# Kernel optimization log

Measured on AMD Instinct MI355X. Metric: run time of the kernel, lower is better.

## Reference

```python
import jax, jax.numpy as jnp
import numpy as np

B, T, N, E = 4, 32, 370, 11840
H, HEADS, DH, L, K = 64, 4, 16, 3, 5

def gelu(x):
    return jax.nn.gelu(x, approximate=False)  # torch default GELU is exact erf

def setup_inputs() -> dict:
    key = jax.random.key(0)
    ks = jax.random.split(key, 18)
    s = 0.05  # keep activations well-scaled
    return {
        "x": jax.random.normal(ks[0], (B, T, N, H), jnp.float32),
        "edge_index": jax.random.randint(ks[1], (2, E), 0, N, dtype=jnp.int32),
        "edge_weight": jax.random.uniform(ks[2], (E,), jnp.float32),
        "W_gcn": jax.random.normal(ks[3], (L, H, H), jnp.float32) * s,
        "b_gcn": jax.random.normal(ks[4], (L, H), jnp.float32) * s,
        "W_gat": jax.random.normal(ks[5], (L, H, HEADS * DH), jnp.float32) * s,
        "att_src": jax.random.normal(ks[6], (L, HEADS, DH), jnp.float32) * s,
        "att_dst": jax.random.normal(ks[7], (L, HEADS, DH), jnp.float32) * s,
        "b_gat": jax.random.normal(ks[8], (L, HEADS * DH), jnp.float32) * s,
        "W_t": jax.random.normal(ks[9], (L, H, H, K), jnp.float32) * s,  # (O,I,K)
        "b_t": jax.random.normal(ks[10], (L, H), jnp.float32) * s,
        "ln_g": jnp.ones((L, H), jnp.float32),
        "ln_b": jnp.zeros((L, H), jnp.float32),
        "W1": jax.random.normal(ks[11], (N * H, 256), jnp.float32) * s,
        "b1": jax.random.normal(ks[12], (256,), jnp.float32) * s,
        "W2": jax.random.normal(ks[13], (256, 64), jnp.float32) * s,
        "b2": jax.random.normal(ks[14], (64,), jnp.float32) * s,
    }

def reference(x, edge_index, edge_weight, W_gcn, b_gcn, W_gat, att_src, att_dst,
              b_gat, W_t, b_t, ln_g, ln_b, W1, b1, W2, b2):
    Bb, Tt, Nn, Ff = x.shape
    G = Bb * Tt
    nL = W_gcn.shape[0]
    heads, dh = att_src.shape[1], att_src.shape[2]
    Hh = heads * dh
    # shared topology across all G graphs; add self-loops (PyG default, fill=1.0)
    src, dst = edge_index[0], edge_index[1]
    loop = jnp.arange(Nn, dtype=src.dtype)
    src2 = jnp.concatenate([src, loop])
    dst2 = jnp.concatenate([dst, loop])
    ew2 = jnp.concatenate([edge_weight, jnp.ones((Nn,), edge_weight.dtype)])
    # symmetric GCN normalization (same for every graph in the batch)
    deg = jnp.zeros((Nn,), x.dtype).at[dst2].add(ew2)
    dis = jnp.where(deg > 0, jax.lax.rsqrt(deg), jnp.zeros_like(deg))
    gnorm = dis[src2] * ew2 * dis[dst2]                       # (E2,)
    h = x.reshape(G, Nn, Ff)
    for l in range(nL):
        # ---- GCNConv: transform -> gather -> weighted scatter-add ----
        hw = h @ W_gcn[l]                                     # (G,N,H)
        msg = hw[:, src2] * gnorm[None, :, None]              # (G,E2,H)
        g = jnp.zeros_like(hw).at[:, dst2].add(msg) + b_gcn[l]
        g = gelu(g)
        # ---- GATConv: per-edge softmax attention over incoming edges ----
        gh = (g @ W_gat[l]).reshape(G, Nn, heads, dh)
        asrc = (gh * att_src[l]).sum(-1)                      # (G,N,heads)
        adst = (gh * att_dst[l]).sum(-1)
        e = jax.nn.leaky_relu(asrc[:, src2] + adst[:, dst2], negative_slope=0.2)
        m = jnp.full((G, Nn, heads), -jnp.inf, e.dtype).at[:, dst2].max(e)
        ex = jnp.exp(e - m[:, dst2])
        den = jnp.zeros((G, Nn, heads), e.dtype).at[:, dst2].add(ex)
        alpha = ex / den[:, dst2]                             # (G,E2,heads)
        msgs = gh[:, src2] * alpha[..., None]                 # (G,E2,heads,dh)
        out = jnp.zeros_like(gh).at[:, dst2].add(msgs).reshape(G, Nn, Hh) + b_gat[l]
        # ---- residual + LayerNorm ----
        r = out + h[..., :Hh]
        mu = r.mean(-1, keepdims=True)
        var = ((r - mu) ** 2).mean(-1, keepdims=True)
        h = (r - mu) * jax.lax.rsqrt(var + 1e-5) * ln_g[l] + ln_b[l]
    # ---- temporal convs over T per (batch, node) ----
    Hc = h.shape[-1]
    xt = h.reshape(Bb, Tt, Nn, Hc).transpose(0, 2, 3, 1).reshape(Bb * Nn, Hc, Tt)
    for l in range(nL):
        c = jax.lax.conv_general_dilated(
            xt, W_t[l], (1,), "SAME", dimension_numbers=("NCH", "OIH", "NCH"))
        xt = gelu(c + b_t[l][None, :, None]) + xt
    z = xt.reshape(Bb, Nn, Hc, Tt).transpose(0, 3, 1, 2).reshape(Bb, Tt, Nn * Hc)
    return gelu(z @ W1 + b1) @ W2 + b2
```

## Files before the change

### kernel.cpp

```cpp
#include <hip/hip_runtime.h>
#include <hip/hip_bf16.h>

#define B_   4
#define T_   32
#define N_   370
#define NP_  384
#define E_   11840
#define E2_  12210
#define H_   64
#define G_   128
#define GN_  47360
#define BN_  1480
#define NH_  23680
#define ECAP 320
#define KCH_ 128
#define NCH_ 185

typedef __hip_bfloat16 bf;
typedef short short8 __attribute__((ext_vector_type(8)));
typedef float f32x4 __attribute__((ext_vector_type(4)));

__device__ __forceinline__ float gelu_f(float x){
  return 0.5f * x * (1.0f + erff(x * 0.7071067811865475f));
}
__device__ __forceinline__ float lrelu(float v){ return v > 0.f ? v : 0.2f * v; }
__device__ __forceinline__ float b2f(bf x){ return __bfloat162float(x); }
__device__ __forceinline__ void store_bf4(bf* p, float4 v){
  bf tmp[4] = {__float2bfloat16(v.x), __float2bfloat16(v.y),
               __float2bfloat16(v.z), __float2bfloat16(v.w)};
  *(ushort4*)p = *(const ushort4*)tmp;
}
__device__ __forceinline__ unsigned pk_bf2(float a, float b){
  bf lo = __float2bfloat16(a), hi = __float2bfloat16(b);
  return (unsigned)*(unsigned short*)&lo | ((unsigned)*(unsigned short*)&hi << 16);
}
__device__ __forceinline__ void load_bf8(const bf* p, float* v){
  uint4 u = *(const uint4*)p;
  unsigned ua[4] = {u.x, u.y, u.z, u.w};
  #pragma unroll
  for (int i = 0; i < 4; ++i){
    v[2*i]   = __uint_as_float(ua[i] << 16);
    v[2*i+1] = __uint_as_float(ua[i] & 0xffff0000u);
  }
}

__global__ __launch_bounds__(1024) void k_degscan(const int* __restrict__ ei,
    const float* __restrict__ ew, float* __restrict__ degG,
    int* __restrict__ offs, int* __restrict__ cursor){
  __shared__ float degS[512];
  __shared__ int cntS[512];
  int tid = threadIdx.x;
  if (tid < 512){ degS[tid] = 0.f; cntS[tid] = 0; }
  __syncthreads();
  for (int e = tid; e < E2_; e += 1024){
    int dst = (e < E_) ? ei[E_ + e] : (e - E_);
    float w = (e < E_) ? ew[e] : 1.0f;
    atomicAdd(&degS[dst], w);
    atomicAdd(&cntS[dst], 1);
  }
  __syncthreads();
  if (tid < N_) degG[tid] = degS[tid];
  if (tid < 64){
    int lane = tid;
    int run = 0;
    for (int c0 = 0; c0 < N_; c0 += 64){
      int n = c0 + lane;
      int v = (n < N_) ? cntS[n] : 0;
      int s = v;
      #pragma unroll
      for (int m = 1; m < 64; m <<= 1){
        int t = __shfl_up(s, m, 64);
        if (lane >= m) s += t;
      }
      int excl = run + s - v;
      if (n < N_){ offs[n] = excl; cursor[n] = excl; }
      run += __shfl(s, 63, 64);
    }
    if (lane == 0) offs[N_] = run;
  }
}

__global__ void k_gfa(const int* __restrict__ ei, const float* __restrict__ ew,
                      const float* __restrict__ deg, int* __restrict__ cursor,
                      int* __restrict__ csr_soff, float* __restrict__ A32){
  int e = blockIdx.x * 256 + threadIdx.x;
  if (e >= E2_) return;
  int s = (e < E_) ? ei[e] : (e - E_);
  int d = (e < E_) ? ei[E_ + e] : (e - E_);
  float w = (e < E_) ? ew[e] : 1.0f;
  float ds = deg[s] > 0.f ? rsqrtf(deg[s]) : 0.f;
  float dd = deg[d] > 0.f ? rsqrtf(deg[d]) : 0.f;
  float gn = ds * w * dd;
  int pos = atomicAdd(&cursor[d], 1);
  csr_soff[pos] = s << 13;
  atomicAdd(&A32[d * NP_ + s], gn);
}

__global__ void k_prep(const float* __restrict__ A32, bf* __restrict__ A16,
                       const float* __restrict__ W_gcn, const float* __restrict__ W_gat,
                       bf* __restrict__ WT, const float* __restrict__ Wt,
                       bf* __restrict__ WB){
  int b = blockIdx.x;
  if (b < 144){
    int i = b * 256 + threadIdx.x;
    float4 v = *(const float4*)&A32[i * 4];
    store_bf4(&A16[i * 4], v);
  } else if (b < 240){
    int i = (b - 144) * 256 + threadIdx.x;
    int ci = i & 63;
    int co = (i >> 6) & 63;
    int m  = (i >> 12) & 1;
    int l  = i >> 13;
    const float* W = m ? W_gat : W_gcn;
    WT[i] = __float2bfloat16(W[(size_t)(l * 64 + ci) * 64 + co]);
  } else {
    int i = (b - 240) * 256 + threadIdx.x;
    int j = i & 7;
    int r = i >> 3;
    int lane = r & 63;
    int mi = (r >> 6) & 3;
    int t2 = r >> 8;
    int kk = t2 % 10, l = t2 / 10;
    int ho = mi * 16 + (lane & 15);
    int k  = kk >> 1;
    int ci = (kk & 1) * 32 + (lane >> 4) * 8 + j;
    WB[i] = __float2bfloat16(Wt[((l * 64 + ho) * 64 + ci) * 5 + k]);
  }
}

__global__ __launch_bounds__(256) void k_gcn_dense(const float* __restrict__ hin,
    const bf* __restrict__ A16, const bf* __restrict__ WT,
    const float* __restrict__ b_gcn, const float* __restrict__ att_s,
    const float* __restrict__ att_d, bf* __restrict__ gh16,
    float* __restrict__ asrc, float* __restrict__ adst){
  __shared__ bf As[64 * 136];
  __shared__ bf Bs[64 * 136];
  __shared__ bf Ws1[64 * 72];
  __shared__ bf Ws2[64 * 72];
  __shared__ bf ts[64 * 72];
  int tid = threadIdx.x;
  int b0 = blockIdx.x;
  int xcd = b0 & 7, jj6 = b0 >> 3;
  int g = xcd * 16 + jj6 / 6;
  int m0 = (jj6 % 6) * 64;
  {
    int u = tid & 7, r0w = tid >> 3;
    #pragma unroll
    for (int it = 0; it < 2; ++it){
      int r = r0w + it * 32;
      *(uint4*)&Ws1[r * 72 + u * 8] = *(const uint4*)&WT[(size_t)r * 64 + u * 8];
      *(uint4*)&Ws2[r * 72 + u * 8] = *(const uint4*)&WT[(size_t)(64 + r) * 64 + u * 8];
    }
  }
  int lane = tid & 63, w = tid >> 6;
  int lr = lane & 15, lg = lane >> 4;
  f32x4 acc[4];
  #pragma unroll
  for (int nt = 0; nt < 4; ++nt){ f32x4 zv = {0.f,0.f,0.f,0.f}; acc[nt] = zv; }
  for (int kc = 0; kc < 3; ++kc){
    int u = tid & 15, r = tid >> 4;
    #pragma unroll
    for (int it = 0; it < 4; ++it){
      int row = it * 16 + r;
      *(uint4*)&As[row * 136 + u * 8] =
          *(const uint4*)&A16[(size_t)(m0 + row) * NP_ + kc * 128 + u * 8];
    }
    #pragma unroll
    for (int it = 0; it < 4; ++it){
      int nn = (it * 16 + r) * 2;
      int n = kc * 128 + nn;
      float4 v0 = (n < N_) ? *(const float4*)&hin[((size_t)g * N_ + n) * 64 + u * 4]
                           : make_float4(0.f, 0.f, 0.f, 0.f);
      float4 v1 = (n + 1 < N_) ? *(const float4*)&hin[((size_t)g * N_ + n + 1) * 64 + u * 4]
                               : make_float4(0.f, 0.f, 0.f, 0.f);
      float a0[4] = {v0.x, v0.y, v0.z, v0.w};
      float a1[4] = {v1.x, v1.y, v1.z, v1.w};
      #pragma unroll
      for (int q = 0; q < 4; ++q)
        *(unsigned*)&Bs[(u * 4 + q) * 136 + nn] = pk_bf2(a0[q], a1[q]);
    }
    __syncthreads();
    #pragma unroll
    for (int ks = 0; ks < 4; ++ks){
      short8 af = *(const short8*)&As[(w * 16 + lr) * 136 + ks * 32 + lg * 8];
      #pragma unroll
      for (int nt = 0; nt < 4; ++nt){
        short8 bfr = *(const short8*)&Bs[(nt * 16 + lr) * 136 + ks * 32 + lg * 8];
        acc[nt] = __builtin_amdgcn_mfma_f32_16x16x32_bf16(af, bfr, acc[nt], 0, 0, 0);
      }
    }
    __syncthreads();
  }
  #pragma unroll
  for (int nt = 0; nt < 4; ++nt)
    #pragma unroll
    for (int q = 0; q < 4; ++q)
      ts[(w * 16 + lg * 4 + q) * 72 + nt * 16 + lr] = __float2bfloat16(acc[nt][q]);
  f32x4 acc2[4];
  #pragma unroll
  for (int nt = 0; nt < 4; ++nt){ f32x4 zv = {0.f,0.f,0.f,0.f}; acc2[nt] = zv; }
  #pragma unroll
  for (int ks = 0; ks < 2; ++ks){
    short8 af = *(const short8*)&ts[(w * 16 + lr) * 72 + ks * 32 + lg * 8];
    #pragma unroll
    for (int nt = 0; nt < 4; ++nt){
      short8 bfr = *(const short8*)&Ws1[(nt * 16 + lr) * 72 + ks * 32 + lg * 8];
      acc2[nt] = __builtin_amdgcn_mfma_f32_16x16x32_bf16(af, bfr, acc2[nt], 0, 0, 0);
    }
  }
  #pragma unroll
  for (int nt = 0; nt < 4; ++nt){
    float bv = b_gcn[nt * 16 + lr];
    #pragma unroll
    for (int q = 0; q < 4; ++q){
      float gv = gelu_f(acc2[nt][q] + bv);
      ts[(w * 16 + lg * 4 + q) * 72 + nt * 16 + lr] = __float2bfloat16(gv);
    }
  }
  f32x4 acc3[4];
  #pragma unroll
  for (int nt = 0; nt < 4; ++nt){ f32x4 zv = {0.f,0.f,0.f,0.f}; acc3[nt] = zv; }
  #pragma unroll
  for (int ks = 0; ks < 2; ++ks){
    short8 af = *(const short8*)&ts[(w * 16 + lr) * 72 + ks * 32 + lg * 8];
    #pragma unroll
    for (int nt = 0; nt < 4; ++nt){
      short8 bfr = *(const short8*)&Ws2[(nt * 16 + lr) * 72 + ks * 32 + lg * 8];
      acc3[nt] = __builtin_amdgcn_mfma_f32_16x16x32_bf16(af, bfr, acc3[nt], 0, 0, 0);
    }
  }
  #pragma unroll
  for (int nt = 0; nt < 4; ++nt){
    float sa = att_s[nt * 16 + lr];
    float sd = att_d[nt * 16 + lr];
    float ps[4], pd[4];
    #pragma unroll
    for (int q = 0; q < 4; ++q){
      int n = m0 + w * 16 + lg * 4 + q;
      if (n < N_)
        gh16[((size_t)n * G_ + g) * 64 + nt * 16 + lr] = __float2bfloat16(acc3[nt][q]);
      ps[q] = acc3[nt][q] * sa;
      pd[q] = acc3[nt][q] * sd;
    }
    #pragma unroll
    for (int q = 0; q < 4; ++q){
      ps[q] += __shfl_xor(ps[q], 1, 64); ps[q] += __shfl_xor(ps[q], 2, 64);
      ps[q] += __shfl_xor(ps[q], 4, 64); ps[q] += __shfl_xor(ps[q], 8, 64);
      pd[q] += __shfl_xor(pd[q], 1, 64); pd[q] += __shfl_xor(pd[q], 2, 64);
      pd[q] += __shfl_xor(pd[q], 4, 64); pd[q] += __shfl_xor(pd[q], 8, 64);
    }
    if (lr == 0){
      #pragma unroll
      for (int q = 0; q < 4; ++q){
        int n = m0 + w * 16 + lg * 4 + q;
        if (n < N_){
          asrc[((size_t)n * G_ + g) * 4 + nt] = ps[q];
          adst[((size_t)n * G_ + g) * 4 + nt] = pd[q];
        }
      }
    }
  }
}

__global__ __launch_bounds__(256) void k_gat_agg(const bf* __restrict__ gh,
    const float* __restrict__ asrc, const float* __restrict__ adst,
    const int* __restrict__ csr_soff, const int* __restrict__ offs,
    const float* __restrict__ b_gat, const float* __restrict__ ln_g,
    const float* __restrict__ ln_b, const float* __restrict__ hin,
    float* __restrict__ hout){
  __shared__ int sS[ECAP];
  int b0 = blockIdx.x;
  int gg = (b0 & 7) >> 1;
  int n = (b0 >> 3) * 2 + (b0 & 1);
  int tid = threadIdx.x;
  int o0 = offs[n], o1 = offs[n + 1];
  int deg = o1 - o0;
  int cap = deg < ECAP ? deg : ECAP;
  for (int i = tid; i < cap; i += 256) sS[i] = csr_soff[o0 + i];
  __syncthreads();
  int ql = tid >> 3, c8 = tid & 7;
  int g = gg * 32 + ql;
  int head = c8 >> 1;
  int gh4 = g * 4 + head;
  int toff = gg * 2048 + ql * 64 + c8 * 8;
  float adv = adst[n * 512 + gh4];
  float den = 0.f;
  float a[8];
  #pragma unroll
  for (int j = 0; j < 8; ++j) a[j] = 0.f;
  int p = 0;
  for (; p + 2 <= cap; p += 2){
    int s0 = sS[p], s1 = sS[p+1];
    float w0 = __expf(lrelu(asrc[(s0 >> 4) + gh4] + adv));
    float w1 = __expf(lrelu(asrc[(s1 >> 4) + gh4] + adv));
    den += w0 + w1;
    float v0[8], v1[8];
    load_bf8(gh + s0 + toff, v0);
    load_bf8(gh + s1 + toff, v1);
    #pragma unroll
    for (int j = 0; j < 8; ++j) a[j] += w0 * v0[j] + w1 * v1[j];
  }
  for (; p < cap; ++p){
    int sv = sS[p];
    float w0 = __expf(lrelu(asrc[(sv >> 4) + gh4] + adv));
    den += w0;
    float v[8];
    load_bf8(gh + sv + toff, v);
    #pragma unroll
    for (int j = 0; j < 8; ++j) a[j] += w0 * v[j];
  }
  for (int r = cap; r < deg; ++r){
    int sv = csr_soff[o0 + r];
    float w0 = __expf(lrelu(asrc[(sv >> 4) + gh4] + adv));
    den += w0;
    float v[8];
    load_bf8(gh + sv + toff, v);
    #pragma unroll
    for (int j = 0; j < 8; ++j) a[j] += w0 * v[j];
  }
  float inv = 1.f / den;
  float4 bg0 = *(const float4*)&b_gat[c8 * 8];
  float4 bg1 = *(const float4*)&b_gat[c8 * 8 + 4];
  float bb[8] = {bg0.x, bg0.y, bg0.z, bg0.w, bg1.x, bg1.y, bg1.z, bg1.w};
  size_t hbase = ((size_t)g * N_ + n) * 64 + c8 * 8;
  float4 h0 = *(const float4*)&hin[hbase];
  float4 h1 = *(const float4*)&hin[hbase + 4];
  float hh[8] = {h0.x, h0.y, h0.z, h0.w, h1.x, h1.y, h1.z, h1.w};
  float r8[8];
  float s1 = 0.f;
  #pragma unroll
  for (int j = 0; j < 8; ++j){
    r8[j] = a[j] * inv + bb[j] + hh[j];
    s1 += r8[j];
  }
  s1 += __shfl_xor(s1, 1, 64); s1 += __shfl_xor(s1, 2, 64); s1 += __shfl_xor(s1, 4, 64);
  float mu = s1 * (1.f / 64.f);
  float s2 = 0.f;
  #pragma unroll
  for (int j = 0; j < 8; ++j){
    float d = r8[j] - mu;
    s2 += d * d;
  }
  s2 += __shfl_xor(s2, 1, 64); s2 += __shfl_xor(s2, 2, 64); s2 += __shfl_xor(s2, 4, 64);
  float rstd = rsqrtf(s2 * (1.f / 64.f) + 1e-5f);
  float4 lg0 = *(const float4*)&ln_g[c8 * 8];
  float4 lg1 = *(const float4*)&ln_g[c8 * 8 + 4];
  float4 lb0 = *(const float4*)&ln_b[c8 * 8];
  float4 lb1 = *(const float4*)&ln_b[c8 * 8 + 4];
  float lg[8] = {lg0.x, lg0.y, lg0.z, lg0.w, lg1.x, lg1.y, lg1.z, lg1.w};
  float lb[8] = {lb0.x, lb0.y, lb0.z, lb0.w, lb1.x, lb1.y, lb1.z, lb1.w};
  float4 w0v, w1v;
  w0v.x = (r8[0]-mu)*rstd*lg[0]+lb[0]; w0v.y = (r8[1]-mu)*rstd*lg[1]+lb[1];
  w0v.z = (r8[2]-mu)*rstd*lg[2]+lb[2]; w0v.w = (r8[3]-mu)*rstd*lg[3]+lb[3];
  w1v.x = (r8[4]-mu)*rstd*lg[4]+lb[4]; w1v.y = (r8[5]-mu)*rstd*lg[5]+lb[5];
  w1v.z = (r8[6]-mu)*rstd*lg[6]+lb[6]; w1v.w = (r8[7]-mu)*rstd*lg[7]+lb[7];
  *(float4*)&hout[hbase] = w0v;
  *(float4*)&hout[hbase + 4] = w1v;
}

__global__ __launch_bounds__(256) void k_wt_tfuse(const float* __restrict__ h,
    const bf* __restrict__ WB, const float* __restrict__ bt,
    bf* __restrict__ z16, const float* __restrict__ W1, bf* __restrict__ W1T){
  __shared__ __align__(16) char smem[17408];
  int tid = threadIdx.x;
  if (blockIdx.x >= BN_){
    float* ts = (float*)smem;
    int bi = blockIdx.x - BN_;
    int k0 = (bi % 370) * 64, c0 = (bi / 370) * 64;
    #pragma unroll
    for (int it = 0; it < 4; ++it){
      int idx = it * 256 + tid;
      int r = idx >> 4, c4 = (idx & 15) * 4;
      *(float4*)&ts[r * 68 + c4] = *(const float4*)&W1[(size_t)(k0 + r) * 256 + c0 + c4];
    }
    __syncthreads();
    #pragma unroll
    for (int it = 0; it < 4; ++it){
      int idx = it * 256 + tid;
      int c = idx >> 4, k4 = (idx & 15) * 4;
      float4 v;
      v.x = ts[(k4 + 0) * 68 + c];
      v.y = ts[(k4 + 1) * 68 + c];
      v.z = ts[(k4 + 2) * 68 + c];
      v.w = ts[(k4 + 3) * 68 + c];
      store_bf4(&W1T[(size_t)(c0 + c) * 23680 + k0 + k4], v);
    }
    return;
  }
  float* xf = (float*)smem;
  char* xTg = smem + 8704;
  int w = tid >> 6, lane = tid & 63;
  int bn = blockIdx.x;
  int b = bn / N_, n = bn - b * N_;
  int lq = lane >> 4, lr = lane & 15;
  #pragma unroll
  for (int r = 0; r < 2; ++r){
    int t = w * 8 + r * 4 + lq;
    int c4 = lr * 4;
    float4 v = *(const float4*)&h[((size_t)(b * T_ + t) * N_ + n) * 64 + c4];
    *(float4*)&xf[t * 68 + c4] = v;
    int row = t + 2;
    bf bv[4] = {__float2bfloat16(v.x), __float2bfloat16(v.y),
                __float2bfloat16(v.z), __float2bfloat16(v.w)};
    int bo = (c4 * 2) ^ ((row & 7) << 4);
    *(uint2*)&xTg[row * 128 + bo] = *(const uint2*)bv;
  }
  if (w == 0){
    int zr = (lq < 2) ? lq : (lq + 32);
    *(uint2*)&xTg[zr * 128 + lr * 8] = make_uint2(0u, 0u);
  }
  __syncthreads();
  for (int l = 0; l < 3; ++l){
    const short8* Wp = (const short8*)(WB + (size_t)l * 20480);
    f32x4 acc[2];
    {
      f32x4 zv = {0.f, 0.f, 0.f, 0.f};
      acc[0] = zv; acc[1] = zv;
    }
    #pragma unroll 2
    for (int kk = 0; kk < 10; ++kk){
      int k = kk >> 1;
      int bbyte = (kk & 1) * 64 + lq * 16;
      short8 bfr[2];
      #pragma unroll
      for (int nj = 0; nj < 2; ++nj){
        int row = nj * 16 + lr + k;
        bfr[nj] = *(const short8*)&xTg[row * 128 + (bbyte ^ ((row & 7) << 4))];
      }
      short8 afr = Wp[(kk * 4 + w) * 64 + lane];
      #pragma unroll
      for (int nj = 0; nj < 2; ++nj)
        acc[nj] = __builtin_amdgcn_mfma_f32_16x16x32_bf16(
            afr, bfr[nj], acc[nj], 0, 0, 0);
    }
    __syncthreads();
    {
      int ho0 = w * 16 + lq * 4;
      float4 bt4 = *(const float4*)&bt[l * 64 + ho0];
      float btv[4] = {bt4.x, bt4.y, bt4.z, bt4.w};
      #pragma unroll
      for (int nj = 0; nj < 2; ++nj){
        int t = nj * 16 + lr;
        float4 xr = *(const float4*)&xf[t * 68 + ho0];
        float xv[4] = {xr.x, xr.y, xr.z, xr.w};
        float ov[4];
        #pragma unroll
        for (int q = 0; q < 4; ++q)
          ov[q] = gelu_f(acc[nj][q] + btv[q]) + xv[q];
        *(float4*)&xf[t * 68 + ho0] = make_float4(ov[0], ov[1], ov[2], ov[3]);
        int row = t + 2;
        bf bvv[4] = {__float2bfloat16(ov[0]), __float2bfloat16(ov[1]),
                     __float2bfloat16(ov[2]), __float2bfloat16(ov[3])};
        *(uint2*)&xTg[row * 128 + ((ho0 * 2) ^ ((row & 7) << 4))] = *(const uint2*)bvv;
      }
    }
    __syncthreads();
  }
  #pragma unroll
  for (int r = 0; r < 2; ++r){
    int t = w * 8 + r * 4 + lq;
    int c4 = lr * 4;
    float4 v = *(const float4*)&xf[t * 68 + c4];
    store_bf4(&z16[(size_t)(b * T_ + t) * NH_ + n * 64 + c4], v);
  }
}

__global__ __launch_bounds__(256) void k_mlp1(const bf* __restrict__ z16,
    const bf* __restrict__ W1T, float* __restrict__ pbuf){
  __shared__ bf zs[128 * 136];
  __shared__ bf ws[128 * 136];
  int kc = blockIdx.x;
  int ch = blockIdx.y;
  int tid = threadIdx.x;
  int k0 = kc * KCH_;
  {
    int u = tid & 15, r = tid >> 4;
    #pragma unroll
    for (int it = 0; it < 8; ++it){
      int row = it * 16 + r;
      uint4 v = *(const uint4*)&z16[(size_t)row * NH_ + k0 + u * 8];
      *(uint4*)&zs[row * 136 + u * 8] = v;
    }
    #pragma unroll
    for (int it = 0; it < 8; ++it){
      int col = it * 16 + r;
      uint4 v = *(const uint4*)&W1T[(size_t)(ch * 128 + col) * 23680 + k0 + u * 8];
      *(uint4*)&ws[col * 136 + u * 8] = v;
    }
  }
  __syncthreads();
  int lane = tid & 63, w = tid >> 6;
  int lr = lane & 15, lg = lane >> 4;
  int wr = w * 32;
  f32x4 acc[2][8];
  #pragma unroll
  for (int mt = 0; mt < 2; ++mt)
    #pragma unroll
    for (int nt = 0; nt < 8; ++nt){
      f32x4 zv = {0.f, 0.f, 0.f, 0.f};
      acc[mt][nt] = zv;
    }
  #pragma unroll
  for (int ks = 0; ks < 4; ++ks){
    short8 af[2], bfr[8];
    #pragma unroll
    for (int mt = 0; mt < 2; ++mt)
      af[mt] = *(const short8*)&zs[(wr + mt * 16 + lr) * 136 + ks * 32 + lg * 8];
    #pragma unroll
    for (int nt = 0; nt < 8; ++nt)
      bfr[nt] = *(const short8*)&ws[(nt * 16 + lr) * 136 + ks * 32 + lg * 8];
    #pragma unroll
    for (int mt = 0; mt < 2; ++mt)
      #pragma unroll
      for (int nt = 0; nt < 8; ++nt)
        acc[mt][nt] = __builtin_amdgcn_mfma_f32_16x16x32_bf16(
            af[mt], bfr[nt], acc[mt][nt], 0, 0, 0);
  }
  float* pb = pbuf + (size_t)kc * 32768 + ch * 128;
  #pragma unroll
  for (int mt = 0; mt < 2; ++mt)
    #pragma unroll
    for (int nt = 0; nt < 8; ++nt){
      int row = wr + mt * 16 + lg * 4;
      int col = nt * 16 + lr;
      #pragma unroll
      for (int q = 0; q < 4; ++q)
        pb[(size_t)(row + q) * 256 + col] = acc[mt][nt][q];
    }
}

__global__ __launch_bounds__(64) void k_mlp2(const float* __restrict__ pbuf,
    const float* __restrict__ b1, const float* __restrict__ W2,
    const float* __restrict__ b2, float* __restrict__ outp){
  __shared__ float a[256];
  int row = blockIdx.x, tid = threadIdx.x;
  const float* p = pbuf + (size_t)row * 256 + tid * 4;
  float sx = 0.f, sy = 0.f, sz = 0.f, sw = 0.f;
  #pragma unroll 5
  for (int kc = 0; kc < NCH_; ++kc){
    float4 v = *(const float4*)&p[(size_t)kc * 32768];
    sx += v.x; sy += v.y; sz += v.z; sw += v.w;
  }
  float4 bv = *(const float4*)&b1[tid * 4];
  a[tid * 4 + 0] = gelu_f(sx + bv.x);
  a[tid * 4 + 1] = gelu_f(sy + bv.y);
  a[tid * 4 + 2] = gelu_f(sz + bv.z);
  a[tid * 4 + 3] = gelu_f(sw + bv.w);
  __syncthreads();
  float acc = b2[tid];
  for (int i = 0; i < 256; ++i) acc += a[i] * W2[i * 64 + tid];
  outp[row * 64 + tid] = acc;
}

extern "C" void kernel_launch(void* const* d_in, const int* in_sizes, int n_in,
                              void* d_out, int out_size, void* d_ws, size_t ws_size,
                              hipStream_t stream){
  const float* x     = (const float*)d_in[0];
  const int*   ei    = (const int*)  d_in[1];
  const float* ew    = (const float*)d_in[2];
  const float* W_gcn = (const float*)d_in[3];
  const float* b_gcn = (const float*)d_in[4];
  const float* W_gat = (const float*)d_in[5];
  const float* att_s = (const float*)d_in[6];
  const float* att_d = (const float*)d_in[7];
  const float* b_gat = (const float*)d_in[8];
  const float* W_t   = (const float*)d_in[9];
  const float* b_t   = (const float*)d_in[10];
  const float* ln_g  = (const float*)d_in[11];
  const float* ln_b  = (const float*)d_in[12];
  const float* W1    = (const float*)d_in[13];
  const float* b1    = (const float*)d_in[14];
  const float* W2    = (const float*)d_in[15];
  const float* b2    = (const float*)d_in[16];
  float* outp = (float*)d_out;

  float* F = (float*)d_ws;
  size_t off = 0;
  float* asrc   = F + off; off += 189440;
  float* adst   = F + off; off += 189440;
  float* degG   = F + off; off += 512;
  float* WTf    = F + off; off += 61440;
  float* h      = F + off; off += 3031040;
  float* bufB   = F + off; off += 3031040;
  float* bufC   = F + off; off += 3031040;
  float* bufD   = F + off; off += 3031040;
  float* pbuf   = F + off; off += (size_t)NCH_ * 32768;
  int* I        = (int*)(F + off);
  int* offs     = I;
  int* cursor   = I + 512;
  int* csr_soff = I + 1024;

  bf* WB     = (bf*)WTf;
  bf* WTT    = (bf*)(WTf + 30720);
  bf* W1T    = (bf*)bufB;
  float* A32 = bufC;
  bf* A16    = (bf*)(bufC + 147456);
  bf* gh16   = (bf*)bufD;
  bf* z16    = (bf*)bufD;

  hipMemsetAsync(A32, 0, (size_t)NP_ * NP_ * sizeof(float), stream);

  k_degscan<<<1, 1024, 0, stream>>>(ei, ew, degG, offs, cursor);
  k_gfa<<<48, 256, 0, stream>>>(ei, ew, degG, cursor, csr_soff, A32);
  k_prep<<<480, 256, 0, stream>>>(A32, A16, W_gcn, W_gat, WTT, W_t, WB);

  for (int l = 0; l < 3; ++l){
    const float* hin = (l == 0) ? x : h;
    k_gcn_dense<<<768, 256, 0, stream>>>(hin, A16, WTT + (size_t)l * 8192,
                                         b_gcn + l * 64, att_s + l * 64, att_d + l * 64,
                                         gh16, asrc, adst);
    k_gat_agg<<<1480, 256, 0, stream>>>(gh16, asrc, adst, csr_soff, offs,
                                        b_gat + l * 64, ln_g + l * 64, ln_b + l * 64,
                                        hin, h);
  }

  k_wt_tfuse<<<2 * BN_, 256, 0, stream>>>(h, WB, b_t, z16, W1, W1T);

  dim3 g1(NCH_, 2);
  k_mlp1<<<g1, 256, 0, stream>>>(z16, W1T, pbuf);
  k_mlp2<<<128, 64, 0, stream>>>(pbuf, b1, W2, b2, outp);
}
```

Before: 309.8 us.

## Fuse setup kernels, drop bf16 staging copies, convert A and W1 on load

The memset moves into k_degscan, and the A32-to-bf16 conversion pass is removed along with k_prep, whose weight transposes are merged into k_gfa. k_gcn_dense now reads fp32 A and packs it to bf16 while filling shared memory. The separate W1 transpose to bf16 is removed, so k_mlp1 loads fp32 W1 directly and transposes and packs it into LDS. k_mlp2 switches to 256 threads with a split reduction. Together these cut launches and intermediate buffer traffic, at the cost of reading W1 and A in fp32 (double the bytes) with strided LDS writes in the hot GEMM loads.

```diff
diff --git a/kernel.cpp b/kernel.cpp
--- a/kernel.cpp
+++ b/kernel.cpp
@@ -46,11 +46,13 @@
 
 __global__ __launch_bounds__(1024) void k_degscan(const int* __restrict__ ei,
     const float* __restrict__ ew, float* __restrict__ degG,
-    int* __restrict__ offs, int* __restrict__ cursor){
+    int* __restrict__ offs, int* __restrict__ cursor, float4* __restrict__ A32v){
   __shared__ float degS[512];
   __shared__ int cntS[512];
   int tid = threadIdx.x;
   if (tid < 512){ degS[tid] = 0.f; cntS[tid] = 0; }
+  for (int i = tid; i < 36864; i += 1024)
+    A32v[i] = make_float4(0.f, 0.f, 0.f, 0.f);
   __syncthreads();
   for (int e = tid; e < E2_; e += 1024){
     int dst = (e < E_) ? ei[E_ + e] : (e - E_);
@@ -82,31 +84,25 @@
 
 __global__ void k_gfa(const int* __restrict__ ei, const float* __restrict__ ew,
                       const float* __restrict__ deg, int* __restrict__ cursor,
-                      int* __restrict__ csr_soff, float* __restrict__ A32){
-  int e = blockIdx.x * 256 + threadIdx.x;
-  if (e >= E2_) return;
-  int s = (e < E_) ? ei[e] : (e - E_);
-  int d = (e < E_) ? ei[E_ + e] : (e - E_);
-  float w = (e < E_) ? ew[e] : 1.0f;
-  float ds = deg[s] > 0.f ? rsqrtf(deg[s]) : 0.f;
-  float dd = deg[d] > 0.f ? rsqrtf(deg[d]) : 0.f;
-  float gn = ds * w * dd;
-  int pos = atomicAdd(&cursor[d], 1);
-  csr_soff[pos] = s << 13;
-  atomicAdd(&A32[d * NP_ + s], gn);
-}
-
-__global__ void k_prep(const float* __restrict__ A32, bf* __restrict__ A16,
-                       const float* __restrict__ W_gcn, const float* __restrict__ W_gat,
-                       bf* __restrict__ WT, const float* __restrict__ Wt,
-                       bf* __restrict__ WB){
+                      int* __restrict__ csr_soff, float* __restrict__ A32,
+                      const float* __restrict__ W_gcn, const float* __restrict__ W_gat,
+                      bf* __restrict__ WT, const float* __restrict__ Wt,
+                      bf* __restrict__ WB){
   int b = blockIdx.x;
-  if (b < 144){
-    int i = b * 256 + threadIdx.x;
-    float4 v = *(const float4*)&A32[i * 4];
-    store_bf4(&A16[i * 4], v);
-  } else if (b < 240){
-    int i = (b - 144) * 256 + threadIdx.x;
+  if (b < 48){
+    int e = b * 256 + threadIdx.x;
+    if (e >= E2_) return;
+    int s = (e < E_) ? ei[e] : (e - E_);
+    int d = (e < E_) ? ei[E_ + e] : (e - E_);
+    float w = (e < E_) ? ew[e] : 1.0f;
+    float ds = deg[s] > 0.f ? rsqrtf(deg[s]) : 0.f;
+    float dd = deg[d] > 0.f ? rsqrtf(deg[d]) : 0.f;
+    float gn = ds * w * dd;
+    int pos = atomicAdd(&cursor[d], 1);
+    csr_soff[pos] = s << 13;
+    atomicAdd(&A32[d * NP_ + s], gn);
+  } else if (b < 144){
+    int i = (b - 48) * 256 + threadIdx.x;
     int ci = i & 63;
     int co = (i >> 6) & 63;
     int m  = (i >> 12) & 1;
@@ -114,7 +110,7 @@
     const float* W = m ? W_gat : W_gcn;
     WT[i] = __float2bfloat16(W[(size_t)(l * 64 + ci) * 64 + co]);
   } else {
-    int i = (b - 240) * 256 + threadIdx.x;
+    int i = (b - 144) * 256 + threadIdx.x;
     int j = i & 7;
     int r = i >> 3;
     int lane = r & 63;
@@ -129,7 +125,7 @@
 }
 
 __global__ __launch_bounds__(256) void k_gcn_dense(const float* __restrict__ hin,
-    const bf* __restrict__ A16, const bf* __restrict__ WT,
+    const float* __restrict__ A32, const bf* __restrict__ WT,
     const float* __restrict__ b_gcn, const float* __restrict__ att_s,
     const float* __restrict__ att_d, bf* __restrict__ gh16,
     float* __restrict__ asrc, float* __restrict__ adst){
@@ -162,8 +158,12 @@
     #pragma unroll
     for (int it = 0; it < 4; ++it){
       int row = it * 16 + r;
-      *(uint4*)&As[row * 136 + u * 8] =
-          *(const uint4*)&A16[(size_t)(m0 + row) * NP_ + kc * 128 + u * 8];
+      const float* ap = &A32[(size_t)(m0 + row) * NP_ + kc * 128 + u * 8];
+      float4 a0 = *(const float4*)ap;
+      float4 a1 = *(const float4*)(ap + 4);
+      uint4 pv = make_uint4(pk_bf2(a0.x, a0.y), pk_bf2(a0.z, a0.w),
+                            pk_bf2(a1.x, a1.y), pk_bf2(a1.z, a1.w));
+      *(uint4*)&As[row * 136 + u * 8] = pv;
     }
     #pragma unroll
     for (int it = 0; it < 4; ++it){
@@ -358,37 +358,13 @@
   *(float4*)&hout[hbase + 4] = w1v;
 }
 
-__global__ __launch_bounds__(256) void k_wt_tfuse(const float* __restrict__ h,
+__global__ __launch_bounds__(256) void k_tfuse(const float* __restrict__ h,
     const bf* __restrict__ WB, const float* __restrict__ bt,
-    bf* __restrict__ z16, const float* __restrict__ W1, bf* __restrict__ W1T){
-  __shared__ __align__(16) char smem[17408];
+    bf* __restrict__ z16){
+  __shared__ float xf[32 * 68];
+  __shared__ float4 xTgv[36 * 8];
+  char* xTg = (char*)xTgv;
   int tid = threadIdx.x;
-  if (blockIdx.x >= BN_){
-    float* ts = (float*)smem;
-    int bi = blockIdx.x - BN_;
-    int k0 = (bi % 370) * 64, c0 = (bi / 370) * 64;
-    #pragma unroll
-    for (int it = 0; it < 4; ++it){
-      int idx = it * 256 + tid;
-      int r = idx >> 4, c4 = (idx & 15) * 4;
-      *(float4*)&ts[r * 68 + c4] = *(const float4*)&W1[(size_t)(k0 + r) * 256 + c0 + c4];
-    }
-    __syncthreads();
-    #pragma unroll
-    for (int it = 0; it < 4; ++it){
-      int idx = it * 256 + tid;
-      int c = idx >> 4, k4 = (idx & 15) * 4;
-      float4 v;
-      v.x = ts[(k4 + 0) * 68 + c];
-      v.y = ts[(k4 + 1) * 68 + c];
-      v.z = ts[(k4 + 2) * 68 + c];
-      v.w = ts[(k4 + 3) * 68 + c];
-      store_bf4(&W1T[(size_t)(c0 + c) * 23680 + k0 + k4], v);
-    }
-    return;
-  }
-  float* xf = (float*)smem;
-  char* xTg = smem + 8704;
   int w = tid >> 6, lane = tid & 63;
   int bn = blockIdx.x;
   int b = bn / N_, n = bn - b * N_;
@@ -466,7 +442,7 @@
 }
 
 __global__ __launch_bounds__(256) void k_mlp1(const bf* __restrict__ z16,
-    const bf* __restrict__ W1T, float* __restrict__ pbuf){
+    const float* __restrict__ W1, float* __restrict__ pbuf){
   __shared__ bf zs[128 * 136];
   __shared__ bf ws[128 * 136];
   int kc = blockIdx.x;
@@ -482,10 +458,19 @@
       *(uint4*)&zs[row * 136 + u * 8] = v;
     }
     #pragma unroll
-    for (int it = 0; it < 8; ++it){
-      int col = it * 16 + r;
-      uint4 v = *(const uint4*)&W1T[(size_t)(ch * 128 + col) * 23680 + k0 + u * 8];
-      *(uint4*)&ws[col * 136 + u * 8] = v;
+    for (int it = 0; it < 4; ++it){
+      int kp = it * 16 + r;
+      const float* w0p = &W1[(size_t)(k0 + kp * 2) * 256 + ch * 128 + u * 8];
+      const float* w1p = w0p + 256;
+      float4 wa0 = *(const float4*)w0p, wa1 = *(const float4*)(w0p + 4);
+      float4 wb0 = *(const float4*)w1p, wb1 = *(const float4*)(w1p + 4);
+      float ca[8] = {wa0.x, wa0.y, wa0.z, wa0.w, wa1.x, wa1.y, wa1.z, wa1.w};
+      float cb[8] = {wb0.x, wb0.y, wb0.z, wb0.w, wb1.x, wb1.y, wb1.z, wb1.w};
+      #pragma unroll
+      for (int q = 0; q < 8; ++q){
+        int col = u * 8 + q;
+        *(unsigned*)&ws[col * 136 + kp * 2] = pk_bf2(ca[q], cb[q]);
+      }
     }
   }
   __syncthreads();
@@ -529,27 +514,33 @@
     }
 }
 
-__global__ __launch_bounds__(64) void k_mlp2(const float* __restrict__ pbuf,
+__global__ __launch_bounds__(256) void k_mlp2(const float* __restrict__ pbuf,
     const float* __restrict__ b1, const float* __restrict__ W2,
     const float* __restrict__ b2, float* __restrict__ outp){
   __shared__ float a[256];
+  __shared__ float red[4][64];
   int row = blockIdx.x, tid = threadIdx.x;
-  const float* p = pbuf + (size_t)row * 256 + tid * 4;
-  float sx = 0.f, sy = 0.f, sz = 0.f, sw = 0.f;
-  #pragma unroll 5
-  for (int kc = 0; kc < NCH_; ++kc){
-    float4 v = *(const float4*)&p[(size_t)kc * 32768];
-    sx += v.x; sy += v.y; sz += v.z; sw += v.w;
-  }
-  float4 bv = *(const float4*)&b1[tid * 4];
-  a[tid * 4 + 0] = gelu_f(sx + bv.x);
-  a[tid * 4 + 1] = gelu_f(sy + bv.y);
-  a[tid * 4 + 2] = gelu_f(sz + bv.z);
-  a[tid * 4 + 3] = gelu_f(sw + bv.w);
+  const float* p = pbuf + (size_t)row * 256 + tid;
+  float s0 = 0.f, s1 = 0.f, s2 = 0.f, s3 = 0.f, s4 = 0.f;
+  for (int kc = 0; kc < NCH_; kc += 5){
+    s0 += p[(size_t)(kc+0) * 32768];
+    s1 += p[(size_t)(kc+1) * 32768];
+    s2 += p[(size_t)(kc+2) * 32768];
+    s3 += p[(size_t)(kc+3) * 32768];
+    s4 += p[(size_t)(kc+4) * 32768];
+  }
+  a[tid] = gelu_f(((s0 + s1) + (s2 + s3)) + s4 + b1[tid]);
   __syncthreads();
-  float acc = b2[tid];
-  for (int i = 0; i < 256; ++i) acc += a[i] * W2[i * 64 + tid];
-  outp[row * 64 + tid] = acc;
+  int w = tid >> 6, lane = tid & 63;
+  float acc = 0.f;
+  #pragma unroll
+  for (int i = 0; i < 64; ++i)
+    acc += a[w * 64 + i] * W2[(w * 64 + i) * 64 + lane];
+  red[w][lane] = acc;
+  __syncthreads();
+  if (tid < 64)
+    outp[row * 64 + tid] = red[0][tid] + red[1][tid] + red[2][tid] + red[3][tid]
+                           + b2[tid];
 }
 
 extern "C" void kernel_launch(void* const* d_in, const int* in_sizes, int n_in,
@@ -581,7 +572,6 @@
   float* degG   = F + off; off += 512;
   float* WTf    = F + off; off += 61440;
   float* h      = F + off; off += 3031040;
-  float* bufB   = F + off; off += 3031040;
   float* bufC   = F + off; off += 3031040;
   float* bufD   = F + off; off += 3031040;
   float* pbuf   = F + off; off += (size_t)NCH_ * 32768;
@@ -592,21 +582,17 @@
 
   bf* WB     = (bf*)WTf;
   bf* WTT    = (bf*)(WTf + 30720);
-  bf* W1T    = (bf*)bufB;
   float* A32 = bufC;
-  bf* A16    = (bf*)(bufC + 147456);
   bf* gh16   = (bf*)bufD;
   bf* z16    = (bf*)bufD;
 
-  hipMemsetAsync(A32, 0, (size_t)NP_ * NP_ * sizeof(float), stream);
-
-  k_degscan<<<1, 1024, 0, stream>>>(ei, ew, degG, offs, cursor);
-  k_gfa<<<48, 256, 0, stream>>>(ei, ew, degG, cursor, csr_soff, A32);
-  k_prep<<<480, 256, 0, stream>>>(A32, A16, W_gcn, W_gat, WTT, W_t, WB);
+  k_degscan<<<1, 1024, 0, stream>>>(ei, ew, degG, offs, cursor, (float4*)A32);
+  k_gfa<<<384, 256, 0, stream>>>(ei, ew, degG, cursor, csr_soff, A32,
+                                 W_gcn, W_gat, WTT, W_t, WB);
 
   for (int l = 0; l < 3; ++l){
     const float* hin = (l == 0) ? x : h;
-    k_gcn_dense<<<768, 256, 0, stream>>>(hin, A16, WTT + (size_t)l * 8192,
+    k_gcn_dense<<<768, 256, 0, stream>>>(hin, A32, WTT + (size_t)l * 8192,
                                          b_gcn + l * 64, att_s + l * 64, att_d + l * 64,
                                          gh16, asrc, adst);
     k_gat_agg<<<1480, 256, 0, stream>>>(gh16, asrc, adst, csr_soff, offs,
@@ -614,9 +600,9 @@
                                         hin, h);
   }
 
-  k_wt_tfuse<<<2 * BN_, 256, 0, stream>>>(h, WB, b_t, z16, W1, W1T);
+  k_tfuse<<<BN_, 256, 0, stream>>>(h, WB, b_t, z16);
 
   dim3 g1(NCH_, 2);
-  k_mlp1<<<g1, 256, 0, stream>>>(z16, W1T, pbuf);
-  k_mlp2<<<128, 64, 0, stream>>>(pbuf, b1, W2, b2, outp);
-}
+  k_mlp1<<<g1, 256, 0, stream>>>(z16, W1, pbuf);
+  k_mlp2<<<128, 256, 0, stream>>>(pbuf, b1, W2, b2, outp);
+}
```

Measured after the change: 308.2 us. About the same (-0.5%).
